# Performance work log

Measured on AMD Instinct MI355X. Metric: run time of the kernel, lower is better.

Reference implementation:

```python
import jax, jax.numpy as jnp
import numpy as np

C = 512
NH = 4
HD = C // NH
G = 32  # min(32, C) and C % 32 == 0
EPS = 1e-5


def setup_inputs() -> dict:
    key = jax.random.key(0)
    ks = jax.random.split(key, 11)
    s = 1.0 / np.sqrt(C)
    return {
        "x": jax.random.normal(ks[0], (16, C, 32, 32), dtype=jnp.float32),
        "gamma": jnp.ones((C,), jnp.float32),
        "beta": jnp.zeros((C,), jnp.float32),
        "wq": jax.random.normal(ks[1], (C, C), jnp.float32) * s,
        "bq": jax.random.normal(ks[2], (C,), jnp.float32) * 0.01,
        "wk": jax.random.normal(ks[3], (C, C), jnp.float32) * s,
        "bk": jax.random.normal(ks[4], (C,), jnp.float32) * 0.01,
        "wv": jax.random.normal(ks[5], (C, C), jnp.float32) * s,
        "bv": jax.random.normal(ks[6], (C,), jnp.float32) * 0.01,
        "wp": jax.random.normal(ks[7], (C, C), jnp.float32) * s,
        "bp": jax.random.normal(ks[8], (C,), jnp.float32) * 0.01,
    }


def _group_norm(x, gamma, beta):
    b, c, h, w = x.shape
    xr = x.reshape(b, G, c // G, h, w)
    mean = xr.mean(axis=(2, 3, 4), keepdims=True)
    var = xr.var(axis=(2, 3, 4), keepdims=True)
    xn = ((xr - mean) * jax.lax.rsqrt(var + EPS)).reshape(b, c, h, w)
    return xn * gamma[None, :, None, None] + beta[None, :, None, None]


def _conv1x1(x, w, b):
    # 1x1 conv == per-position channel GEMM
    return jnp.einsum('oc,bchw->bohw', w, x) + b[None, :, None, None]


def reference(x, gamma, beta, wq, bq, wk, bk, wv, bv, wp, bp):
    b, c, h, w = x.shape
    hw = h * w
    scale = HD ** (-0.5)
    hn = _group_norm(x, gamma, beta)
    q = _conv1x1(hn, wq, bq).reshape(b, NH, HD, hw)
    k = _conv1x1(hn, wk, bk).reshape(b, NH, HD, hw)
    v = _conv1x1(hn, wv, bv).reshape(b, NH, HD, hw)
    attn = jnp.einsum('bhdq,bhdk->bhqk', q, k) * scale  # [b, nh, hw, hw]
    attn = jax.nn.softmax(attn, axis=-1)
    out = jnp.einsum('bhqk,bhdk->bhdq', attn, v)  # [b, nh, hd, hw]
    out = out.reshape(b, c, h, w)
    out = _conv1x1(out, wp, bp)
    return x + out
```

## Files before the change

### kernel.cpp

```cpp
#include <hip/hip_runtime.h>
#include <math.h>

#define CCH 512
#define NH 4
#define HD 128
#define HW 1024
#define BATCH 16
#define EPS 1e-5f

typedef __attribute__((ext_vector_type(8))) short bfrag;
typedef __attribute__((ext_vector_type(4))) float f4;
typedef __attribute__((ext_vector_type(16))) float f16v;

static __device__ __forceinline__ unsigned short f2bf(float f) {
  union { float f; unsigned u; } v;
  v.f = f;
  unsigned r = v.u + 0x7fff + ((v.u >> 16) & 1);
  return (unsigned short)(r >> 16);
}
static __device__ __forceinline__ unsigned pack2(unsigned short a, unsigned short b) {
  return (unsigned)a | ((unsigned)b << 16);
}
static __device__ __forceinline__ unsigned cvt_pk_bf16(float a, float b) {
  unsigned r;
  asm("v_cvt_pk_bf16_f32 %0, %1, %2" : "=v"(r) : "v"(a), "v"(b));
  return r;
}
#if defined(__has_builtin) && __has_builtin(__builtin_amdgcn_exp2f)
#define EXP2(x) __builtin_amdgcn_exp2f(x)
#else
#define EXP2(x) __expf((x) * 0.6931471805599453f)
#endif
static __device__ __forceinline__ void ldg_lds16(const unsigned short* g,
                                                 unsigned short* l) {
  __builtin_amdgcn_global_load_lds(
      (const __attribute__((address_space(1))) unsigned int*)g,
      (__attribute__((address_space(3))) unsigned int*)l, 16, 0, 0);
}

#define QSCALE (0.08838834764831845f * 1.4426950408889634f)

__global__ __launch_bounds__(256) void wcvt_kernel(const float* __restrict__ s0,
                                                   const float* __restrict__ s1,
                                                   const float* __restrict__ s2,
                                                   const float* __restrict__ s3,
                                                   unsigned short* __restrict__ d) {
  const float* srcs[4] = {s0, s1, s2, s3};
  const float* s = srcs[blockIdx.y];
  unsigned short* dp = d + (size_t)blockIdx.y * CCH * CCH;
  int i = blockIdx.x * 256 + threadIdx.x;
  f4 v = ((const f4*)s)[i];
  ushort4 o;
  o.x = f2bf(v.x); o.y = f2bf(v.y); o.z = f2bf(v.z); o.w = f2bf(v.w);
  ((ushort4*)dp)[i] = o;
}

__global__ __launch_bounds__(256) void gn_kernel(const float* __restrict__ x,
                                                 const float* __restrict__ gamma,
                                                 const float* __restrict__ beta,
                                                 unsigned short* __restrict__ hn) {
  int b = blockIdx.x >> 5, g = blockIdx.x & 31;
  const float* xp = x + ((size_t)b * CCH + g * 16) * HW;
  int t = threadIdx.x;
  float s = 0.f, ss = 0.f;
  const f4* xp4 = (const f4*)xp;
  f4 vv[16];
#pragma unroll
  for (int c = 0; c < 16; ++c) {
    f4 v = xp4[c * 256 + t];
    vv[c] = v;
    s += v.x + v.y + v.z + v.w;
    ss += v.x * v.x + v.y * v.y + v.z * v.z + v.w * v.w;
  }
#pragma unroll
  for (int off = 32; off > 0; off >>= 1) {
    s += __shfl_xor(s, off);
    ss += __shfl_xor(ss, off);
  }
  __shared__ float rs[4], rss[4];
  int w = t >> 6;
  if ((t & 63) == 0) { rs[w] = s; rss[w] = ss; }
  __syncthreads();
  s = rs[0] + rs[1] + rs[2] + rs[3];
  ss = rss[0] + rss[1] + rss[2] + rss[3];
  const float invn = 1.f / (16 * HW);
  float mean = s * invn;
  float var = ss * invn - mean * mean;
  float rstd = rsqrtf(var + EPS);
  float a_[16], b_[16];
#pragma unroll
  for (int c = 0; c < 16; ++c) {
    float gm = gamma[g * 16 + c] * rstd;
    a_[c] = gm;
    b_[c] = beta[g * 16 + c] - mean * gm;
  }
#pragma unroll
  for (int i = 0; i < 4; ++i) {
    int p = 4 * t + i;
    uint4 u0, u1;
    u0.x = cvt_pk_bf16(vv[0][i] * a_[0] + b_[0], vv[1][i] * a_[1] + b_[1]);
    u0.y = cvt_pk_bf16(vv[2][i] * a_[2] + b_[2], vv[3][i] * a_[3] + b_[3]);
    u0.z = cvt_pk_bf16(vv[4][i] * a_[4] + b_[4], vv[5][i] * a_[5] + b_[5]);
    u0.w = cvt_pk_bf16(vv[6][i] * a_[6] + b_[6], vv[7][i] * a_[7] + b_[7]);
    u1.x = cvt_pk_bf16(vv[8][i] * a_[8] + b_[8], vv[9][i] * a_[9] + b_[9]);
    u1.y = cvt_pk_bf16(vv[10][i] * a_[10] + b_[10], vv[11][i] * a_[11] + b_[11]);
    u1.z = cvt_pk_bf16(vv[12][i] * a_[12] + b_[12], vv[13][i] * a_[13] + b_[13]);
    u1.w = cvt_pk_bf16(vv[14][i] * a_[14] + b_[14], vv[15][i] * a_[15] + b_[15]);
    unsigned short* dst = hn + ((size_t)b * HW + p) * CCH + g * 16;
    *(uint4*)dst = u0;
    *(uint4*)(dst + 8) = u1;
  }
}

template <int PROJ>
__global__ __launch_bounds__(256, 3) void mm_kernel(
    const unsigned short* __restrict__ Xt, const unsigned short* __restrict__ Wb,
    const float* __restrict__ b0, const float* __restrict__ b1,
    const float* __restrict__ b2, const float* __restrict__ resid,
    unsigned short* __restrict__ O0, unsigned short* __restrict__ O1,
    unsigned short* __restrict__ O2, float* __restrict__ Ofp) {
  int b = blockIdx.z;
  int p0 = blockIdx.x * 128;
  int c0g = blockIdx.y * 128;
  __shared__ __align__(16) unsigned short Xs[128 * 32];
  __shared__ __align__(16) unsigned short Ws[128 * 32];
  int t = threadIdx.x;
  int w = t >> 6, lane = t & 63, l15 = lane & 15, quad = lane >> 4;
  int wp = (w & 1) * 64, wc = (w >> 1) * 64;
  const unsigned short* Xb = Xt + (size_t)b * HW * CCH;
  const unsigned short* Wr = Wb + (size_t)c0g * CCH;
  f4 acc[4][4] = {};
  for (int k0 = 0; k0 < CCH; k0 += 32) {
    __syncthreads();
#pragma unroll
    for (int j = 0; j < 2; ++j) {
      int chk = w * 2 + j;
      int r = chk * 16 + (lane >> 2);
      int c = (lane & 3) ^ (r & 3);
      ldg_lds16(&Xb[(size_t)(p0 + r) * CCH + k0 + c * 8], &Xs[chk * 512]);
      ldg_lds16(&Wr[(size_t)r * CCH + k0 + c * 8], &Ws[chk * 512]);
    }
    __syncthreads();
    bfrag af[4], bf[4];
#pragma unroll
    for (int pt = 0; pt < 4; ++pt) {
      int r = wp + pt * 16 + l15;
      af[pt] = *(const bfrag*)&Xs[r * 32 + (quad ^ (r & 3)) * 8];
    }
#pragma unroll
    for (int ct = 0; ct < 4; ++ct) {
      int r = wc + ct * 16 + l15;
      bf[ct] = *(const bfrag*)&Ws[r * 32 + (quad ^ (r & 3)) * 8];
    }
#pragma unroll
    for (int pt = 0; pt < 4; ++pt)
#pragma unroll
      for (int ct = 0; ct < 4; ++ct)
        acc[pt][ct] = __builtin_amdgcn_mfma_f32_16x16x32_bf16(
            af[pt], bf[ct], acc[pt][ct], 0, 0, 0);
  }
  if (PROJ) {
#pragma unroll
    for (int ct = 0; ct < 4; ++ct) {
      int ch = c0g + wc + ct * 16 + l15;
      float bi = b0[ch];
#pragma unroll
      for (int pt = 0; pt < 4; ++pt) {
        int pos = p0 + wp + pt * 16 + quad * 4;
        f4 v = acc[pt][ct];
        size_t off = (size_t)b * CCH * HW + (size_t)ch * HW + pos;
        float4 rv = *(const float4*)&resid[off];
        float4 st;
        st.x = v.x + bi + rv.x; st.y = v.y + bi + rv.y;
        st.z = v.z + bi + rv.z; st.w = v.w + bi + rv.w;
        *(float4*)&Ofp[off] = st;
      }
    }
  } else {
    int mat = c0g >> 9;
    int c0 = c0g & 511;
    const float* bias = mat == 0 ? b0 : (mat == 1 ? b1 : b2);
    unsigned short* O = mat == 0 ? O0 : (mat == 1 ? O1 : O2);
    const float sc = (mat == 0) ? QSCALE : 1.0f;
#pragma unroll
    for (int ct = 0; ct < 4; ++ct) {
      int ch = c0 + wc + ct * 16 + l15;
      float bi = bias[ch];
#pragma unroll
      for (int pt = 0; pt < 4; ++pt) {
        int pos = p0 + wp + pt * 16 + quad * 4;
        f4 v = acc[pt][ct];
        if (mat < 2) {
          unsigned short* Op = O + (size_t)b * HW * CCH;
          Op[(size_t)(pos + 0) * CCH + ch] = f2bf((v.x + bi) * sc);
          Op[(size_t)(pos + 1) * CCH + ch] = f2bf((v.y + bi) * sc);
          Op[(size_t)(pos + 2) * CCH + ch] = f2bf((v.z + bi) * sc);
          Op[(size_t)(pos + 3) * CCH + ch] = f2bf((v.w + bi) * sc);
        } else {
          unsigned short* Op = O + (size_t)b * CCH * HW;
          ushort4 st;
          st.x = f2bf(v.x + bi); st.y = f2bf(v.y + bi);
          st.z = f2bf(v.z + bi); st.w = f2bf(v.w + bi);
          *(ushort4*)&Op[(size_t)ch * HW + pos] = st;
        }
      }
    }
  }
}

__global__ __launch_bounds__(512, 4) void attn_kernel(
    const unsigned short* __restrict__ Qt, const unsigned short* __restrict__ Kt,
    const unsigned short* __restrict__ Vc, unsigned short* __restrict__ Ot) {
  int bh = blockIdx.x;
  int b = bh >> 2, h = bh & 3;
  int q0 = blockIdx.y * 128;
  int t = threadIdx.x;
  int w = t >> 6, lane = t & 63;
  int l31 = lane & 31, half = lane >> 5;
  int qg = w & 3, kh = w >> 2;
  __shared__ __align__(16) unsigned short S_[32768];
  int q = q0 + qg * 32 + l31;
  const unsigned short* Kbase = Kt + (size_t)b * HW * CCH + h * HD;
  const unsigned short* Vbase = Vc + ((size_t)b * CCH + h * HD) * HW;
  bfrag qf[8];
#pragma unroll
  for (int ks = 0; ks < 8; ++ks)
    qf[ks] = *(const bfrag*)&Qt[((size_t)b * HW + q) * CCH + h * HD +
                                ks * 16 + half * 8];
  f16v o[4] = {};
  float ls[4] = {};
  auto stage = [&](int kt, int bi) {
    int kk0 = kt * 64;
    unsigned short* Kd = S_ + bi * 8192;
    unsigned short* Vd = S_ + 16384 + bi * 8192;
#pragma unroll
    for (int j = 0; j < 2; ++j) {
      int chk = w * 2 + j;
      {
        int r = chk * 4 + (lane >> 4);
        int c = (lane & 15) ^ (r & 15);
        ldg_lds16(&Kbase[(size_t)(kk0 + r) * CCH + c * 8], Kd + chk * 512);
      }
      {
        int r = chk * 8 + (lane >> 3);
        int c = (lane & 7) ^ (r & 7);
        ldg_lds16(&Vbase[(size_t)r * HW + kk0 + c * 8], Vd + chk * 512);
      }
    }
  };
  stage(0, 0);
  for (int kt = 0; kt < 16; ++kt) {
    __syncthreads();
    if (kt < 15) stage(kt + 1, (kt + 1) & 1);
    const unsigned short* K_ = S_ + (kt & 1) * 8192;
    const unsigned short* V_ = S_ + 16384 + (kt & 1) * 8192;
    f16v S = {};
    __builtin_amdgcn_s_setprio(1);
#pragma unroll
    for (int ks = 0; ks < 8; ++ks) {
      int c16 = ks * 2 + half;
      int r = kh * 32 + l31;
      bfrag kf = *(const bfrag*)&K_[r * 128 + ((c16 ^ (r & 15)) << 3)];
      S = __builtin_amdgcn_mfma_f32_32x32x16_bf16(kf, qf[ks], S, 0, 0, 0);
    }
    __builtin_amdgcn_s_setprio(0);
    unsigned pd[8];
#pragma unroll
    for (int i = 0; i < 8; ++i) {
      float p0 = EXP2(S[2 * i]);
      float p1 = EXP2(S[2 * i + 1]);
      ls[i & 3] += p0 + p1;
      pd[i] = cvt_pk_bf16(p0, p1);
    }
#pragma unroll
    for (int s = 0; s < 2; ++s) {
      unsigned a0 = pd[s * 4 + 0], a1 = pd[s * 4 + 1];
      unsigned c0 = pd[s * 4 + 2], c1 = pd[s * 4 + 3];
      asm("v_permlane32_swap_b32 %0, %1" : "+v"(a0), "+v"(c0));
      asm("v_permlane32_swap_b32 %0, %1" : "+v"(a1), "+v"(c1));
      union { unsigned u[4]; bfrag f; } pf;
      pf.u[0] = a0; pf.u[1] = a1; pf.u[2] = c0; pf.u[3] = c1;
      int c8 = (kh * 2 + s) * 2 + half;
      __builtin_amdgcn_s_setprio(1);
#pragma unroll
      for (int dt = 0; dt < 4; ++dt) {
        int r = dt * 32 + l31;
        bfrag vf = *(const bfrag*)&V_[r * 64 + ((c8 ^ (r & 7)) << 3)];
        o[dt] = __builtin_amdgcn_mfma_f32_32x32x16_bf16(vf, pf.f, o[dt],
                                                        0, 0, 0);
      }
      __builtin_amdgcn_s_setprio(0);
    }
  }
  float lrow = (ls[0] + ls[1]) + (ls[2] + ls[3]);
  lrow += __shfl_xor(lrow, 32);
  __syncthreads();
  float* lb = (float*)S_;
  if (kh == 1 && half == 0) lb[qg * 32 + l31] = lrow;
  __syncthreads();
  if (kh == 0) lrow += lb[qg * 32 + l31];
  __syncthreads();
  float* ob = (float*)S_;
  if (kh == 1) {
#pragma unroll
    for (int dt = 0; dt < 4; ++dt) {
      union { f16v v; f4 q4[4]; } u; u.v = o[dt];
#pragma unroll
      for (int rg = 0; rg < 4; ++rg) {
        int d4 = dt * 8 + rg * 2 + half;
        *(f4*)&ob[qg * 4096 + l31 * 128 + ((d4 ^ (l31 & 7)) << 2)] = u.q4[rg];
      }
    }
  }
  __syncthreads();
  if (kh == 0) {
    float inv = 1.f / lrow;
    unsigned short* Op = Ot + ((size_t)b * HW + q) * CCH + h * HD;
#pragma unroll
    for (int dt = 0; dt < 4; ++dt) {
      union { f16v v; f4 q4[4]; } u; u.v = o[dt];
#pragma unroll
      for (int rg = 0; rg < 4; ++rg) {
        int d4 = dt * 8 + rg * 2 + half;
        f4 oth = *(const f4*)&ob[qg * 4096 + l31 * 128 +
                                 ((d4 ^ (l31 & 7)) << 2)];
        f4 mine = u.q4[rg];
        int d = d4 << 2;
        uint2 st;
        st.x = cvt_pk_bf16((mine.x + oth.x) * inv, (mine.y + oth.y) * inv);
        st.y = cvt_pk_bf16((mine.z + oth.z) * inv, (mine.w + oth.w) * inv);
        *(uint2*)&Op[d] = st;
      }
    }
  }
}

extern "C" void kernel_launch(void* const* d_in, const int* in_sizes, int n_in,
                              void* d_out, int out_size, void* d_ws,
                              size_t ws_size, hipStream_t stream) {
  const float* x = (const float*)d_in[0];
  const float* gamma = (const float*)d_in[1];
  const float* beta = (const float*)d_in[2];
  const float* wq = (const float*)d_in[3];
  const float* bq = (const float*)d_in[4];
  const float* wk = (const float*)d_in[5];
  const float* bk = (const float*)d_in[6];
  const float* wv = (const float*)d_in[7];
  const float* bv = (const float*)d_in[8];
  const float* wp = (const float*)d_in[9];
  const float* bp = (const float*)d_in[10];

  const size_t TS = (size_t)BATCH * HW * CCH;
  unsigned short* wB = (unsigned short*)d_ws;
  unsigned short* hn = wB + (size_t)4 * CCH * CCH;
  unsigned short* Qt = hn + TS;
  unsigned short* Kt = Qt + TS;
  unsigned short* Vc = Kt + TS;
  unsigned short* Ot = hn;

  wcvt_kernel<<<dim3(256, 4), 256, 0, stream>>>(wq, wk, wv, wp, wB);
  gn_kernel<<<dim3(BATCH * 32), 256, 0, stream>>>(x, gamma, beta, hn);
  mm_kernel<0><<<dim3(8, 12, BATCH), 256, 0, stream>>>(
      hn, wB, bq, bk, bv, nullptr, Qt, Kt, Vc, nullptr);
  attn_kernel<<<dim3(64, 8), 512, 0, stream>>>(Qt, Kt, Vc, Ot);
  mm_kernel<1><<<dim3(8, 4, BATCH), 256, 0, stream>>>(
      Ot, wB + (size_t)3 * CCH * CCH, bp, bp, bp, x, nullptr, nullptr, nullptr,
      (float*)d_out);
}
```

Baseline: 247.5 us.

## Shrink attention blocks to 64 queries and single-buffer V with mid-iteration wait

The attention kernel now uses 256-thread blocks covering 64 queries each, with twice as many blocks in the grid. K stays double-buffered, but V goes into a single buffer: it is loaded at the start of each iteration and waited on with a partial vmcnt plus a barrier just before the PV MFMAs. This cuts shared memory per block so more blocks fit per CU, and it overlaps the V load with QK and the exp step. The row-sum reduction is folded into the output-combine phase, which removes two barriers. In exchange, each block re-reads K/V for fewer queries, so total K/V traffic doubles, and each iteration gains an extra barrier.

```diff
diff --git a/kernel.cpp b/kernel.cpp
--- a/kernel.cpp
+++ b/kernel.cpp
@@ -208,17 +208,17 @@
   }
 }
 
-__global__ __launch_bounds__(512, 4) void attn_kernel(
+__global__ __launch_bounds__(256, 3) void attn_kernel(
     const unsigned short* __restrict__ Qt, const unsigned short* __restrict__ Kt,
     const unsigned short* __restrict__ Vc, unsigned short* __restrict__ Ot) {
   int bh = blockIdx.x;
   int b = bh >> 2, h = bh & 3;
-  int q0 = blockIdx.y * 128;
+  int q0 = blockIdx.y * 64;
   int t = threadIdx.x;
   int w = t >> 6, lane = t & 63;
   int l31 = lane & 31, half = lane >> 5;
-  int qg = w & 3, kh = w >> 2;
-  __shared__ __align__(16) unsigned short S_[32768];
+  int qg = w & 1, kh = w >> 1;
+  __shared__ __align__(16) unsigned short S_[24576];
   int q = q0 + qg * 32 + l31;
   const unsigned short* Kbase = Kt + (size_t)b * HW * CCH + h * HD;
   const unsigned short* Vbase = Vc + ((size_t)b * CCH + h * HD) * HW;
@@ -229,31 +229,34 @@
                                 ks * 16 + half * 8];
   f16v o[4] = {};
   float ls[4] = {};
-  auto stage = [&](int kt, int bi) {
+  auto stageK = [&](int kt, int bi) {
     int kk0 = kt * 64;
     unsigned short* Kd = S_ + bi * 8192;
-    unsigned short* Vd = S_ + 16384 + bi * 8192;
-#pragma unroll
-    for (int j = 0; j < 2; ++j) {
-      int chk = w * 2 + j;
-      {
-        int r = chk * 4 + (lane >> 4);
-        int c = (lane & 15) ^ (r & 15);
-        ldg_lds16(&Kbase[(size_t)(kk0 + r) * CCH + c * 8], Kd + chk * 512);
-      }
-      {
-        int r = chk * 8 + (lane >> 3);
-        int c = (lane & 7) ^ (r & 7);
-        ldg_lds16(&Vbase[(size_t)r * HW + kk0 + c * 8], Vd + chk * 512);
-      }
+#pragma unroll
+    for (int j = 0; j < 4; ++j) {
+      int chk = w * 4 + j;
+      int r = chk * 4 + (lane >> 4);
+      int c = (lane & 15) ^ (r & 15);
+      ldg_lds16(&Kbase[(size_t)(kk0 + r) * CCH + c * 8], Kd + chk * 512);
     }
   };
-  stage(0, 0);
+  auto stageV = [&](int kt) {
+    int kk0 = kt * 64;
+    unsigned short* Vd = S_ + 16384;
+#pragma unroll
+    for (int j = 0; j < 4; ++j) {
+      int chk = w * 4 + j;
+      int r = chk * 8 + (lane >> 3);
+      int c = (lane & 7) ^ (r & 7);
+      ldg_lds16(&Vbase[(size_t)r * HW + kk0 + c * 8], Vd + chk * 512);
+    }
+  };
+  stageK(0, 0);
   for (int kt = 0; kt < 16; ++kt) {
     __syncthreads();
-    if (kt < 15) stage(kt + 1, (kt + 1) & 1);
+    stageV(kt);
+    if (kt < 15) stageK(kt + 1, (kt + 1) & 1);
     const unsigned short* K_ = S_ + (kt & 1) * 8192;
-    const unsigned short* V_ = S_ + 16384 + (kt & 1) * 8192;
     f16v S = {};
     __builtin_amdgcn_s_setprio(1);
 #pragma unroll
@@ -272,6 +275,13 @@
       ls[i & 3] += p0 + p1;
       pd[i] = cvt_pk_bf16(p0, p1);
     }
+    if (kt < 15)
+      asm volatile("s_waitcnt vmcnt(4)" ::: "memory");
+    else
+      asm volatile("s_waitcnt vmcnt(0)" ::: "memory");
+    __builtin_amdgcn_s_barrier();
+    __builtin_amdgcn_sched_barrier(0);
+    const unsigned short* V_ = S_ + 16384;
 #pragma unroll
     for (int s = 0; s < 2; ++s) {
       unsigned a0 = pd[s * 4 + 0], a1 = pd[s * 4 + 1];
@@ -295,13 +305,10 @@
   float lrow = (ls[0] + ls[1]) + (ls[2] + ls[3]);
   lrow += __shfl_xor(lrow, 32);
   __syncthreads();
-  float* lb = (float*)S_;
-  if (kh == 1 && half == 0) lb[qg * 32 + l31] = lrow;
-  __syncthreads();
-  if (kh == 0) lrow += lb[qg * 32 + l31];
-  __syncthreads();
   float* ob = (float*)S_;
+  float* lb = (float*)S_ + 8192;
   if (kh == 1) {
+    if (half == 0) lb[qg * 32 + l31] = lrow;
 #pragma unroll
     for (int dt = 0; dt < 4; ++dt) {
       union { f16v v; f4 q4[4]; } u; u.v = o[dt];
@@ -314,6 +321,7 @@
   }
   __syncthreads();
   if (kh == 0) {
+    lrow += lb[qg * 32 + l31];
     float inv = 1.f / lrow;
     unsigned short* Op = Ot + ((size_t)b * HW + q) * CCH + h * HD;
 #pragma unroll
@@ -362,7 +370,7 @@
   gn_kernel<<<dim3(BATCH * 32), 256, 0, stream>>>(x, gamma, beta, hn);
   mm_kernel<0><<<dim3(8, 12, BATCH), 256, 0, stream>>>(
       hn, wB, bq, bk, bv, nullptr, Qt, Kt, Vc, nullptr);
-  attn_kernel<<<dim3(64, 8), 512, 0, stream>>>(Qt, Kt, Vc, Ot);
+  attn_kernel<<<dim3(64, 16), 256, 0, stream>>>(Qt, Kt, Vc, Ot);
   mm_kernel<1><<<dim3(8, 4, BATCH), 256, 0, stream>>>(
       Ot, wB + (size_t)3 * CCH * CCH, bp, bp, bp, x, nullptr, nullptr, nullptr,
       (float*)d_out);
```

New measurement: 219.6 us. -11.3%, faster.
